# Kernel optimization log

Measured on AMD Instinct MI355X. Metric: run time of the kernel, lower is better.

The kernel has to match this reference:

```python
import jax, jax.numpy as jnp
import numpy as np

NUM_LONGTERM_MEM = 16  # config.num_longterm_mem


def setup_inputs() -> dict:
    key = jax.random.key(0)
    ks = jax.random.split(key, 9)
    B, T, C, H = 32, 2048, 768, 1536
    s = 0.02
    return {
        "x": jax.random.normal(ks[0], (B, T, C), jnp.float32),
        "Wq": jax.random.normal(ks[1], (C, C), jnp.float32) * s,
        "bq": jax.random.normal(ks[2], (C,), jnp.float32) * s,
        "W0": jax.random.normal(ks[3], (B, H, C), jnp.float32) * s,
        "b0": jax.random.normal(ks[4], (B, H), jnp.float32) * s,
        "W1": jax.random.normal(ks[5], (B, C, H), jnp.float32) * s,
        "b1": jax.random.normal(ks[6], (B, C), jnp.float32) * s,
        "Wo": jax.random.normal(ks[7], (C, C), jnp.float32) * s,
        "bo": jax.random.normal(ks[8], (C,), jnp.float32) * s,
    }


def reference(x, Wq, bq, W0, b0, W1, b1, Wo, bo):
    # x: [B, T, C]. Per-sample memory MLP weights W0 [B,H,C], W1 [B,C,H].
    B, T, C = x.shape
    L = NUM_LONGTERM_MEM
    # query projection (nn.Linear: x @ W^T + b)
    q = jnp.einsum("btc,dc->btd", x, Wq) + bq                       # [B,T,C]
    # per-sample 2-layer memory MLP with SiLU
    h = jax.nn.silu(jnp.einsum("btc,bhc->bth", q, W0) + b0[:, None, :])  # [B,T,H]
    mem = jnp.einsum("bth,bch->btc", h, W1) + b1[:, None, :]        # [B,T,C]
    # adaptive_avg_pool1d over T -> L (T divisible by L => uniform window mean)
    pooled = mem.reshape(B, L, T // L, C).mean(axis=2)              # [B,L,C]
    # output projection
    return jnp.einsum("blc,dc->bld", pooled, Wo) + bo               # [B,L,C]
```

## Files before the change

### kernel.cpp

```cpp
#include <hip/hip_runtime.h>
#include <stdint.h>

#define B_ 32
#define T_ 2048
#define C_ 768
#define H_ 1536
#define L_ 16

typedef unsigned short u16;
typedef __bf16 bf16x8 __attribute__((ext_vector_type(8)));
typedef float f32x4 __attribute__((ext_vector_type(4)));

__device__ __forceinline__ u16 f2bf(float f) {
    union { float f; uint32_t u; } v; v.f = f;
    uint32_t r = (v.u + 0x7fffu + ((v.u >> 16) & 1u)) >> 16;
    return (u16)r;
}

__device__ __forceinline__ float wave_sum(float v) {
    v += __shfl_xor(v, 1);  v += __shfl_xor(v, 2);  v += __shfl_xor(v, 4);
    v += __shfl_xor(v, 8);  v += __shfl_xor(v, 16); v += __shfl_xor(v, 32);
    return v;
}

__global__ void k_cvt(const float* __restrict__ in, u16* __restrict__ out, int n4) {
    int stride = gridDim.x * blockDim.x;
    for (int i = blockIdx.x * blockDim.x + threadIdx.x; i < n4; i += stride) {
        float4 v = reinterpret_cast<const float4*>(in)[i];
        ushort4 o;
        o.x = f2bf(v.x); o.y = f2bf(v.y); o.z = f2bf(v.z); o.w = f2bf(v.w);
        reinterpret_cast<ushort4*>(out)[i] = o;
    }
}

__global__ void k_cvt3(const float* __restrict__ s0, u16* __restrict__ d0, int n0,
                       const float* __restrict__ s1, u16* __restrict__ d1, int n1,
                       const float* __restrict__ s2, u16* __restrict__ d2, int n2,
                       int e0, int e1) {
    const float* s; u16* d; int n, b0, nb;
    if (blockIdx.x < (unsigned)e0)      { s = s0; d = d0; n = n0; b0 = 0;  nb = e0; }
    else if (blockIdx.x < (unsigned)e1) { s = s1; d = d1; n = n1; b0 = e0; nb = e1 - e0; }
    else                      { s = s2; d = d2; n = n2; b0 = e1; nb = gridDim.x - e1; }
    int stride = nb * blockDim.x;
    for (int i = (blockIdx.x - b0) * blockDim.x + threadIdx.x; i < n; i += stride) {
        float4 v = reinterpret_cast<const float4*>(s)[i];
        ushort4 o;
        o.x = f2bf(v.x); o.y = f2bf(v.y); o.z = f2bf(v.z); o.w = f2bf(v.w);
        reinterpret_cast<ushort4*>(d)[i] = o;
    }
}

__device__ __forceinline__ void gload16(const u16* g, u16* l) {
    __builtin_amdgcn_global_load_lds((const __attribute__((address_space(1))) void*)g,
                                     (__attribute__((address_space(3))) void*)l, 16, 0, 0);
}

template <int EPI>
__global__ __launch_bounds__(512, 2) void k_gemm9(const u16* __restrict__ Aall,
                                                  const u16* __restrict__ Ball,
                                                  const float* __restrict__ biasall,
                                                  u16* __restrict__ qout,
                                                  float* __restrict__ ph) {
    __shared__ u16 sm[81920];
    const int t = threadIdx.x;
    const int w = t >> 6, lane = t & 63;
    const int wr = w >> 2, wc = w & 3;
    const int l15 = lane & 15, kq = lane >> 4, cx = lane & 7;

    const int gx = gridDim.x, gy = gridDim.y;
    const int nwg = gx * gy * gridDim.z;
    int flat = blockIdx.x + gx * (blockIdx.y + gy * blockIdx.z);
    if ((nwg & 7) == 0) flat = (flat & 7) * (nwg >> 3) + (flat >> 3);
    const int bx = flat % gx;
    const int tmp = flat / gx;
    const int by = tmp % gy;
    const int bz = tmp / gy;

    const int n0 = bx * 256;
    const int m0 = by * 256;
    const u16* A; const u16* Bm; const float* bias;
    if constexpr (EPI == 0) {
        A = Aall + (size_t)m0 * C_;
        Bm = Ball + (size_t)n0 * C_;
        bias = biasall + n0;
    } else {
        A = Aall + ((size_t)bz * T_ + m0) * C_;
        Bm = Ball + ((size_t)bz * H_ + n0) * C_;
        bias = biasall + (size_t)bz * H_ + n0;
    }

    const int rl = (w << 4) + (lane >> 3);
    const int cs = (((lane & 7) ^ ((lane >> 3) & 7)) << 3);
    const int ldst = (w << 10);

    auto stA = [&](int kt, int buf) {
#pragma unroll
        for (int h = 0; h < 2; ++h) {
            const u16* g = A + (size_t)(h * 128 + rl) * C_ + kt * 64 + cs;
            u16* l = sm + buf * 16384 + h * 8192 + ldst;
            gload16(g, l);
            gload16(g + 8 * C_, l + 512);
        }
    };
    auto stB = [&](int kt, int buf) {
#pragma unroll
        for (int h = 0; h < 2; ++h) {
            const u16* g = Bm + (size_t)(h * 128 + rl) * C_ + kt * 64 + cs;
            u16* l = sm + 49152 + buf * 16384 + h * 8192 + ldst;
            gload16(g, l);
            gload16(g + 8 * C_, l + 512);
        }
    };

    f32x4 acc[8][4];
#pragma unroll
    for (int m = 0; m < 8; ++m)
#pragma unroll
        for (int n = 0; n < 4; ++n) acc[m][n] = (f32x4){0.f, 0.f, 0.f, 0.f};

    bf16x8 a0[4][2], a1[4][2], bfr[2][2];

    const int koff0 = ((kq ^ cx) << 3);
    const int koff1 = (((4 + kq) ^ cx) << 3);
    const u16* aB0 = sm + wr * 8192 + l15 * 64 + koff0;
    const u16* aB1 = sm + wr * 8192 + l15 * 64 + koff1;
    const u16* bB0 = sm + 49152 + (wc >> 1) * 8192 + (wc & 1) * 4096 + l15 * 64 + koff0;
    const u16* bB1 = sm + 49152 + (wc >> 1) * 8192 + (wc & 1) * 4096 + l15 * 64 + koff1;

    auto rdB0 = [&](int off) {
        bfr[0][0] = *reinterpret_cast<const bf16x8*>(bB0 + off);
        bfr[1][0] = *reinterpret_cast<const bf16x8*>(bB0 + off + 1024);
        bfr[0][1] = *reinterpret_cast<const bf16x8*>(bB1 + off);
        bfr[1][1] = *reinterpret_cast<const bf16x8*>(bB1 + off + 1024);
    };
    auto rdB1 = [&](int off) {
        bfr[0][0] = *reinterpret_cast<const bf16x8*>(bB0 + off + 2048);
        bfr[1][0] = *reinterpret_cast<const bf16x8*>(bB0 + off + 3072);
        bfr[0][1] = *reinterpret_cast<const bf16x8*>(bB1 + off + 2048);
        bfr[1][1] = *reinterpret_cast<const bf16x8*>(bB1 + off + 3072);
    };
    auto rdA0 = [&](int off) {
#pragma unroll
        for (int mm = 0; mm < 4; ++mm) {
            a0[mm][0] = *reinterpret_cast<const bf16x8*>(aB0 + off + mm * 1024);
            a0[mm][1] = *reinterpret_cast<const bf16x8*>(aB1 + off + mm * 1024);
        }
    };
    auto rdA1 = [&](int off) {
#pragma unroll
        for (int mm = 0; mm < 4; ++mm) {
            a1[mm][0] = *reinterpret_cast<const bf16x8*>(aB0 + off + 4096 + mm * 1024);
            a1[mm][1] = *reinterpret_cast<const bf16x8*>(aB1 + off + 4096 + mm * 1024);
        }
    };
    auto mma16 = [&](bf16x8 (&a)[4][2], int mq, int qn) {
        __builtin_amdgcn_s_setprio(1);
#pragma unroll
        for (int ks = 0; ks < 2; ++ks)
#pragma unroll
            for (int mm = 0; mm < 4; ++mm)
#pragma unroll
                for (int nn = 0; nn < 2; ++nn)
                    acc[mq * 4 + mm][qn * 2 + nn] = __builtin_amdgcn_mfma_f32_16x16x32_bf16(
                        a[mm][ks], bfr[nn][ks], acc[mq * 4 + mm][qn * 2 + nn], 0, 0, 0);
        __builtin_amdgcn_s_setprio(0);
    };

    stA(0, 0); stB(0, 0); stA(1, 1);
    asm volatile("s_waitcnt vmcnt(4)" ::: "memory");
    __builtin_amdgcn_s_barrier();

    int ba = 0;
#pragma unroll 1
    for (int kt = 0; kt < 12; ++kt) {
        const int bb = kt & 1;
        int ban = ba + 2; if (ban >= 3) ban -= 3;
        const bool s2 = (kt + 2 < 12);
        if (kt + 1 < 12) stB(kt + 1, bb ^ 1);
        if (s2) stA(kt + 2, ban);
        const int aoff = ba * 16384;
        const int boff = bb * 16384;
        rdB0(boff);
        rdA0(aoff);
        rdA1(aoff);
        mma16(a0, 0, 0);
        mma16(a1, 1, 0);
        __builtin_amdgcn_sched_barrier(0);
        rdB1(boff);
        mma16(a0, 0, 1);
        mma16(a1, 1, 1);
        if (s2) asm volatile("s_waitcnt vmcnt(4)" ::: "memory");
        else    asm volatile("s_waitcnt vmcnt(0)" ::: "memory");
        __builtin_amdgcn_s_barrier();
        ba = (ba + 1 == 3) ? 0 : ba + 1;
    }

    if constexpr (EPI == 0) {
        const int colb = n0 + wc * 64 + l15;
        const int rowb = m0 + wr * 128 + (kq << 2);
        float bv[4];
#pragma unroll
        for (int n = 0; n < 4; ++n) bv[n] = bias[wc * 64 + n * 16 + l15];
#pragma unroll
        for (int m = 0; m < 8; ++m)
#pragma unroll
            for (int r = 0; r < 4; ++r) {
                size_t ro = (size_t)(rowb + m * 16 + r) * C_;
#pragma unroll
                for (int n = 0; n < 4; ++n)
                    qout[ro + colb + n * 16] = f2bf(acc[m][n][r] + bv[n]);
            }
    } else {
        const int lwin = by * 2 + wr;
#pragma unroll
        for (int n = 0; n < 4; ++n) {
            int cloc = wc * 64 + n * 16 + l15;
            float bv = bias[cloc];
            float s = 0.f;
#pragma unroll
            for (int m = 0; m < 8; ++m)
#pragma unroll
                for (int r = 0; r < 4; ++r) {
                    float v = acc[m][n][r] + bv;
                    s += v / (1.f + __expf(-v));
                }
            s += __shfl_xor(s, 16);
            s += __shfl_xor(s, 32);
            if (kq == 0)
                ph[((size_t)bz * L_ + lwin) * H_ + n0 + cloc] = s * (1.f / 128.f);
        }
    }
}

__device__ __forceinline__ void stage_bf16_gload(const u16* gtile, int ld, u16* Ts,
                                                 int w, int lane) {
    const int r_in = lane >> 3;
    const int c0   = (lane & 7) << 3;
#pragma unroll
    for (int j = 0; j < 4; ++j) {
        int row = ((w << 2) + j) * 8 + r_in;
        const u16* g = gtile + (size_t)row * ld + c0;
        u16* l = Ts + (((w << 2) + j) << 9);
        gload16(g, l);
    }
}

__device__ __forceinline__ void stage_f32_cvt(const float* gtile, int ld, u16* Ts, int t) {
#pragma unroll
    for (int i = 0; i < 8; ++i) {
        int slot = t + (i << 8);
        int row  = slot >> 4;
        int c4   = (slot & 15) << 2;
        float4 v = *reinterpret_cast<const float4*>(gtile + (size_t)row * ld + c4);
        ushort4 o;
        o.x = f2bf(v.x); o.y = f2bf(v.y); o.z = f2bf(v.z); o.w = f2bf(v.w);
        *reinterpret_cast<ushort4*>(&Ts[row * 64 + c4]) = o;
    }
}

__device__ __forceinline__ void mfma_tile(const u16* As, const u16* Bs,
                                          f32x4 (&acc)[4][4], int wr, int wc, int lane) {
#pragma unroll
    for (int ks = 0; ks < 2; ++ks) {
        const int ko = (ks << 5) + ((lane >> 4) << 3);
        bf16x8 a[4], b[4];
#pragma unroll
        for (int m = 0; m < 4; ++m)
            a[m] = *reinterpret_cast<const bf16x8*>(&As[(wr * 64 + m * 16 + (lane & 15)) * 64 + ko]);
#pragma unroll
        for (int n = 0; n < 4; ++n)
            b[n] = *reinterpret_cast<const bf16x8*>(&Bs[(wc * 64 + n * 16 + (lane & 15)) * 64 + ko]);
#pragma unroll
        for (int m = 0; m < 4; ++m)
#pragma unroll
            for (int n = 0; n < 4; ++n)
                acc[m][n] = __builtin_amdgcn_mfma_f32_16x16x32_bf16(a[m], b[n], acc[m][n], 0, 0, 0);
    }
}

__global__ __launch_bounds__(256, 2) void k_gemm1(const float* __restrict__ x,
                                                  const u16* __restrict__ Wqb,
                                                  const float* __restrict__ bq,
                                                  u16* __restrict__ qb) {
    __shared__ u16 As[128 * 64];
    __shared__ u16 Bs[128 * 64];
    const int t = threadIdx.x, w = t >> 6, lane = t & 63;
    const int wr = w >> 1, wc = w & 1;
    const int m0 = blockIdx.y * 128;
    const int n0 = blockIdx.x * 128;

    f32x4 acc[4][4];
#pragma unroll
    for (int m = 0; m < 4; ++m)
#pragma unroll
        for (int n = 0; n < 4; ++n) acc[m][n] = (f32x4){0.f, 0.f, 0.f, 0.f};

    for (int kt = 0; kt < C_ / 64; ++kt) {
        stage_f32_cvt(x + (size_t)m0 * C_ + kt * 64, C_, As, t);
        stage_bf16_gload(Wqb + (size_t)n0 * C_ + kt * 64, C_, Bs, w, lane);
        __syncthreads();
        mfma_tile(As, Bs, acc, wr, wc, lane);
        __syncthreads();
    }

    const int r0 = m0 + wr * 64 + ((lane >> 4) << 2);
    const int cb = n0 + wc * 64 + (lane & 15);
#pragma unroll
    for (int n = 0; n < 4; ++n) {
        int c = cb + n * 16;
        float bb = bq[c];
#pragma unroll
        for (int m = 0; m < 4; ++m)
#pragma unroll
            for (int r = 0; r < 4; ++r)
                qb[(size_t)(r0 + m * 16 + r) * C_ + c] = f2bf(acc[m][n][r] + bb);
    }
}

template <bool BPRE>
__global__ __launch_bounds__(256, 2) void k_gemm2(const u16* __restrict__ qb,
                                                  const u16* __restrict__ W0b,
                                                  const float* __restrict__ W0f,
                                                  const float* __restrict__ b0,
                                                  float* __restrict__ ph) {
    __shared__ u16 As[128 * 64];
    __shared__ u16 Bs[128 * 64];
    __shared__ float Ps[2][128];
    const int t = threadIdx.x, w = t >> 6, lane = t & 63;
    const int wr = w >> 1, wc = w & 1;
    const int b  = blockIdx.z;
    const int mt = blockIdx.y;
    const int n0 = blockIdx.x * 128;
    const u16* Abase = qb + ((size_t)b * T_ + mt * 128) * C_;

    f32x4 acc[4][4];
#pragma unroll
    for (int m = 0; m < 4; ++m)
#pragma unroll
        for (int n = 0; n < 4; ++n) acc[m][n] = (f32x4){0.f, 0.f, 0.f, 0.f};

    for (int kt = 0; kt < C_ / 64; ++kt) {
        stage_bf16_gload(Abase + kt * 64, C_, As, w, lane);
        if (BPRE)
            stage_bf16_gload(W0b + ((size_t)b * H_ + n0) * C_ + kt * 64, C_, Bs, w, lane);
        else
            stage_f32_cvt(W0f + ((size_t)b * H_ + n0) * C_ + kt * 64, C_, Bs, t);
        __syncthreads();
        mfma_tile(As, Bs, acc, wr, wc, lane);
        __syncthreads();
    }

    float s[4];
#pragma unroll
    for (int n = 0; n < 4; ++n) {
        int c = n0 + wc * 64 + n * 16 + (lane & 15);
        float bb = b0[b * H_ + c];
        float sum = 0.f;
#pragma unroll
        for (int m = 0; m < 4; ++m)
#pragma unroll
            for (int r = 0; r < 4; ++r) {
                float v = acc[m][n][r] + bb;
                sum += v / (1.f + __expf(-v));
            }
        sum += __shfl_xor(sum, 16);
        sum += __shfl_xor(sum, 32);
        s[n] = sum;
    }
    if (lane < 16) {
#pragma unroll
        for (int n = 0; n < 4; ++n) Ps[wr][wc * 64 + n * 16 + lane] = s[n];
    }
    __syncthreads();
    if (t < 128)
        ph[((size_t)b * L_ + mt) * H_ + n0 + t] = (Ps[0][t] + Ps[1][t]) * (1.f / 128.f);
}

__global__ __launch_bounds__(256) void k_3a(const float* __restrict__ ph,
                                            const float* __restrict__ W1,
                                            const float* __restrict__ b1,
                                            float* __restrict__ pooled) {
    const int t = threadIdx.x, w = t >> 6, lane = t & 63;
    const int b  = blockIdx.y;
    const int cb = blockIdx.x * 16 + w * 4;

    float acc[4][16];
#pragma unroll
    for (int g = 0; g < 4; ++g)
#pragma unroll
        for (int l = 0; l < 16; ++l) acc[g][l] = 0.f;

    for (int i = 0; i < H_ / 256; ++i) {
        int h0 = i * 256 + lane * 4;
        float4 wv[4];
#pragma unroll
        for (int g = 0; g < 4; ++g)
            wv[g] = *reinterpret_cast<const float4*>(W1 + ((size_t)b * C_ + cb + g) * H_ + h0);
#pragma unroll
        for (int l = 0; l < 16; ++l) {
            float4 pv = *reinterpret_cast<const float4*>(ph + ((size_t)b * L_ + l) * H_ + h0);
#pragma unroll
            for (int g = 0; g < 4; ++g)
                acc[g][l] += wv[g].x * pv.x + wv[g].y * pv.y + wv[g].z * pv.z + wv[g].w * pv.w;
        }
    }
#pragma unroll
    for (int g = 0; g < 4; ++g)
#pragma unroll
        for (int l = 0; l < 16; ++l) acc[g][l] = wave_sum(acc[g][l]);

    if (lane < 16) {
#pragma unroll
        for (int g = 0; g < 4; ++g)
            pooled[((size_t)b * L_ + lane) * C_ + cb + g] = acc[g][lane] + b1[b * C_ + cb + g];
    }
}

__global__ __launch_bounds__(256) void k_3b(const float* __restrict__ pooled,
                                            const float* __restrict__ Wo,
                                            const float* __restrict__ bo,
                                            float* __restrict__ out) {
    __shared__ __align__(16) float ps[4 * 768];
    const int t = threadIdx.x, w = t >> 6, lane = t & 63;
    const int rr0 = blockIdx.x * 4;

    for (int idx = t; idx < 4 * 768; idx += 256)
        ps[idx] = pooled[(size_t)rr0 * 768 + idx];
    __syncthreads();

    for (int d = w; d < 768; d += 4) {
        float a0 = 0.f, a1 = 0.f, a2 = 0.f, a3 = 0.f;
#pragma unroll
        for (int i = 0; i < 3; ++i) {
            int c = i * 256 + lane * 4;
            float4 wv = *reinterpret_cast<const float4*>(Wo + (size_t)d * 768 + c);
            float4 p0 = *reinterpret_cast<const float4*>(&ps[0 * 768 + c]);
            float4 p1 = *reinterpret_cast<const float4*>(&ps[1 * 768 + c]);
            float4 p2 = *reinterpret_cast<const float4*>(&ps[2 * 768 + c]);
            float4 p3 = *reinterpret_cast<const float4*>(&ps[3 * 768 + c]);
            a0 += wv.x * p0.x + wv.y * p0.y + wv.z * p0.z + wv.w * p0.w;
            a1 += wv.x * p1.x + wv.y * p1.y + wv.z * p1.z + wv.w * p1.w;
            a2 += wv.x * p2.x + wv.y * p2.y + wv.z * p2.z + wv.w * p2.w;
            a3 += wv.x * p3.x + wv.y * p3.y + wv.z * p3.z + wv.w * p3.w;
        }
        a0 = wave_sum(a0); a1 = wave_sum(a1); a2 = wave_sum(a2); a3 = wave_sum(a3);
        if (lane == 0) {
            float bb = bo[d];
            out[(size_t)(rr0 + 0) * 768 + d] = a0 + bb;
            out[(size_t)(rr0 + 1) * 768 + d] = a1 + bb;
            out[(size_t)(rr0 + 2) * 768 + d] = a2 + bb;
            out[(size_t)(rr0 + 3) * 768 + d] = a3 + bb;
        }
    }
}

extern "C" void kernel_launch(void* const* d_in, const int* in_sizes, int n_in,
                              void* d_out, int out_size, void* d_ws, size_t ws_size,
                              hipStream_t stream) {
    const float* x  = (const float*)d_in[0];
    const float* Wq = (const float*)d_in[1];
    const float* bq = (const float*)d_in[2];
    const float* W0 = (const float*)d_in[3];
    const float* b0 = (const float*)d_in[4];
    const float* W1 = (const float*)d_in[5];
    const float* b1 = (const float*)d_in[6];
    const float* Wo = (const float*)d_in[7];
    const float* bo = (const float*)d_in[8];
    float* out = (float*)d_out;

    char* p = (char*)d_ws;
    size_t off = 0;
    auto carve = [&](size_t bytes) -> char* {
        char* r = p + off;
        off += (bytes + 255) & ~(size_t)255;
        return r;
    };
    u16*   qb     = (u16*)carve((size_t)B_ * T_ * C_ * 2);
    u16*   Wqb    = (u16*)carve((size_t)C_ * C_ * 2);
    float* ph     = (float*)carve((size_t)B_ * L_ * H_ * 4);
    float* pooled = (float*)carve((size_t)B_ * L_ * C_ * 4);

    const size_t xb_bytes  = (size_t)B_ * T_ * C_ * 2;
    const size_t w0b_bytes = (size_t)B_ * H_ * C_ * 2;

    const int n4x  = B_ * T_ * C_ / 4;
    const int n4wq = C_ * C_ / 4;
    const int n4w0 = B_ * H_ * C_ / 4;

    if (off + xb_bytes + w0b_bytes <= ws_size) {
        u16* xb  = (u16*)carve(xb_bytes);
        u16* W0b = (u16*)carve(w0b_bytes);
        k_cvt3<<<dim3(3072), 256, 0, stream>>>(x, xb, n4x, Wq, Wqb, n4wq,
                                               W0, W0b, n4w0, 1744, 1768);
        k_gemm9<0><<<dim3(C_ / 256, (B_ * T_) / 256), 512, 0, stream>>>(xb, Wqb, bq, qb, nullptr);
        k_gemm9<1><<<dim3(H_ / 256, T_ / 256, B_), 512, 0, stream>>>(qb, W0b, b0, nullptr, ph);
    } else if (off + xb_bytes <= ws_size) {
        u16* xb  = (u16*)carve(xb_bytes);
        u16* W0b = xb;
        k_cvt3<<<dim3(3072), 256, 0, stream>>>(x, xb, n4x, Wq, Wqb, n4wq,
                                               nullptr, nullptr, 0, 3040, 3072);
        k_gemm9<0><<<dim3(C_ / 256, (B_ * T_) / 256), 512, 0, stream>>>(xb, Wqb, bq, qb, nullptr);
        k_cvt<<<dim3(2048), 256, 0, stream>>>(W0, W0b, n4w0);
        k_gemm9<1><<<dim3(H_ / 256, T_ / 256, B_), 512, 0, stream>>>(qb, W0b, b0, nullptr, ph);
    } else {
        u16* W0b = nullptr;
        if (off + w0b_bytes <= ws_size) W0b = (u16*)carve(w0b_bytes);

        k_cvt<<<dim3(64), 256, 0, stream>>>(Wq, Wqb, n4wq);
        if (W0b)
            k_cvt<<<dim3(2048), 256, 0, stream>>>(W0, W0b, n4w0);
        k_gemm1<<<dim3(C_ / 128, (B_ * T_) / 128), 256, 0, stream>>>(x, Wqb, bq, qb);
        if (W0b)
            k_gemm2<true><<<dim3(H_ / 128, L_, B_), 256, 0, stream>>>(qb, W0b, nullptr, b0, ph);
        else
            k_gemm2<false><<<dim3(H_ / 128, L_, B_), 256, 0, stream>>>(qb, nullptr, W0, b0, ph);
    }

    k_3a<<<dim3(C_ / 16, B_), 256, 0, stream>>>(ph, W1, b1, pooled);
    k_3b<<<dim3(B_ * L_ / 4), 256, 0, stream>>>(pooled, Wo, bo, out);
}
```

Before: 623.8 us.

## Fold query projection into per-sample W0 to skip the q GEMM

Uses associativity to precompute Wf = W0·Wq per sample and b0' = b0 + W0·bq. The first layer then runs directly on x, so the large B·T×C×C query GEMM and the q round-trip through memory go away. The price is a new per-sample C×C weight-fusion GEMM (B·H·C·C), a transposed Wq copy, and extra workspace for Wfb. Rounding Wf to bf16 also changes the numerics slightly.

```diff
diff --git a/kernel.cpp b/kernel.cpp
--- a/kernel.cpp
+++ b/kernel.cpp
@@ -33,20 +33,60 @@
     }
 }
 
-__global__ void k_cvt3(const float* __restrict__ s0, u16* __restrict__ d0, int n0,
-                       const float* __restrict__ s1, u16* __restrict__ d1, int n1,
-                       const float* __restrict__ s2, u16* __restrict__ d2, int n2,
-                       int e0, int e1) {
-    const float* s; u16* d; int n, b0, nb;
-    if (blockIdx.x < (unsigned)e0)      { s = s0; d = d0; n = n0; b0 = 0;  nb = e0; }
-    else if (blockIdx.x < (unsigned)e1) { s = s1; d = d1; n = n1; b0 = e0; nb = e1 - e0; }
-    else                      { s = s2; d = d2; n = n2; b0 = e1; nb = gridDim.x - e1; }
-    int stride = nb * blockDim.x;
-    for (int i = (blockIdx.x - b0) * blockDim.x + threadIdx.x; i < n; i += stride) {
-        float4 v = reinterpret_cast<const float4*>(s)[i];
-        ushort4 o;
-        o.x = f2bf(v.x); o.y = f2bf(v.y); o.z = f2bf(v.z); o.w = f2bf(v.w);
-        reinterpret_cast<ushort4*>(d)[i] = o;
+__global__ void k_prep(const float* __restrict__ x, u16* __restrict__ xb, int n4x,
+                       const float* __restrict__ Wq, u16* __restrict__ WqTb,
+                       const float* __restrict__ W0, u16* __restrict__ W0b,
+                       const float* __restrict__ bq, const float* __restrict__ b0,
+                       float* __restrict__ b0f, int e0, int e1) {
+    const int t = threadIdx.x;
+    if (blockIdx.x < (unsigned)e0) {
+        int stride = e0 * 256;
+        for (int i = blockIdx.x * 256 + t; i < n4x; i += stride) {
+            float4 v = reinterpret_cast<const float4*>(x)[i];
+            ushort4 o;
+            o.x = f2bf(v.x); o.y = f2bf(v.y); o.z = f2bf(v.z); o.w = f2bf(v.w);
+            reinterpret_cast<ushort4*>(xb)[i] = o;
+        }
+    } else if (blockIdx.x < (unsigned)e1) {
+        __shared__ u16 tl[64 * 65];
+        const int nb = e1 - e0;
+        for (int tile = blockIdx.x - e0; tile < 144; tile += nb) {
+            int d0 = (tile / 12) * 64, c0 = (tile % 12) * 64;
+            __syncthreads();
+#pragma unroll
+            for (int p = 0; p < 16; ++p) {
+                int idx = p * 256 + t;
+                int r = idx >> 6, c = idx & 63;
+                tl[r * 65 + c] = f2bf(Wq[(size_t)(d0 + r) * 768 + c0 + c]);
+            }
+            __syncthreads();
+#pragma unroll
+            for (int p = 0; p < 16; ++p) {
+                int idx = p * 256 + t;
+                int r = idx >> 6, c = idx & 63;
+                WqTb[(size_t)(c0 + r) * 768 + d0 + c] = tl[c * 65 + r];
+            }
+        }
+    } else {
+        const int w = t >> 6, lane = t & 63;
+        const int nWaves = (gridDim.x - e1) * 4;
+        const float4* bq4 = reinterpret_cast<const float4*>(bq);
+        for (int rr = (blockIdx.x - e1) * 4 + w; rr < B_ * H_; rr += nWaves) {
+            const float4* src = reinterpret_cast<const float4*>(W0 + (size_t)rr * 768);
+            ushort4* dst = reinterpret_cast<ushort4*>(W0b + (size_t)rr * 768);
+            float dot = 0.f;
+#pragma unroll
+            for (int p = 0; p < 3; ++p) {
+                float4 v = src[p * 64 + lane];
+                float4 b4 = bq4[p * 64 + lane];
+                ushort4 o;
+                o.x = f2bf(v.x); o.y = f2bf(v.y); o.z = f2bf(v.z); o.w = f2bf(v.w);
+                dst[p * 64 + lane] = o;
+                dot += v.x * b4.x + v.y * b4.y + v.z * b4.z + v.w * b4.w;
+            }
+            dot = wave_sum(dot);
+            if (lane == 0) b0f[rr] = b0[rr] + dot;
+        }
     }
 }
 
@@ -232,6 +272,155 @@
     }
 }
 
+__global__ __launch_bounds__(512, 2) void k_wf(const u16* __restrict__ W0b,
+                                               const u16* __restrict__ WqTb,
+                                               u16* __restrict__ Wfb) {
+    __shared__ u16 sm[81920];
+    const int t = threadIdx.x;
+    const int w = t >> 6, lane = t & 63;
+    const int wr = w >> 2, wc = w & 3;
+    const int l15 = lane & 15, kq = lane >> 4, cx = lane & 7;
+
+    const int gx = gridDim.x, gy = gridDim.y;
+    const int nwg = gx * gy * gridDim.z;
+    int flat = blockIdx.x + gx * (blockIdx.y + gy * blockIdx.z);
+    if ((nwg & 7) == 0) flat = (flat & 7) * (nwg >> 3) + (flat >> 3);
+    const int bx = flat % gx;
+    const int tmp = flat / gx;
+    const int by = tmp % gy;
+    const int bz = tmp / gy;
+
+    const int n0 = bx * 256;
+    const int m0 = by * 256;
+    const u16* A = W0b + ((size_t)bz * H_ + m0) * C_;
+    const u16* Bm = WqTb + (size_t)n0 * C_;
+
+    const int rl = (w << 4) + (lane >> 3);
+    const int cs = (((lane & 7) ^ ((lane >> 3) & 7)) << 3);
+    const int ldst = (w << 10);
+
+    auto stA = [&](int kt, int buf) {
+#pragma unroll
+        for (int h = 0; h < 2; ++h) {
+            const u16* g = A + (size_t)(h * 128 + rl) * C_ + kt * 64 + cs;
+            u16* l = sm + buf * 16384 + h * 8192 + ldst;
+            gload16(g, l);
+            gload16(g + 8 * C_, l + 512);
+        }
+    };
+    auto stB = [&](int kt, int buf) {
+#pragma unroll
+        for (int h = 0; h < 2; ++h) {
+            const u16* g = Bm + (size_t)(h * 128 + rl) * C_ + kt * 64 + cs;
+            u16* l = sm + 49152 + buf * 16384 + h * 8192 + ldst;
+            gload16(g, l);
+            gload16(g + 8 * C_, l + 512);
+        }
+    };
+
+    f32x4 acc[8][4];
+#pragma unroll
+    for (int m = 0; m < 8; ++m)
+#pragma unroll
+        for (int n = 0; n < 4; ++n) acc[m][n] = (f32x4){0.f, 0.f, 0.f, 0.f};
+
+    bf16x8 a0[4][2], a1[4][2], bfr[2][2];
+
+    const int koff0 = ((kq ^ cx) << 3);
+    const int koff1 = (((4 + kq) ^ cx) << 3);
+    const u16* aB0 = sm + wr * 8192 + l15 * 64 + koff0;
+    const u16* aB1 = sm + wr * 8192 + l15 * 64 + koff1;
+    const u16* bB0 = sm + 49152 + (wc >> 1) * 8192 + (wc & 1) * 4096 + l15 * 64 + koff0;
+    const u16* bB1 = sm + 49152 + (wc >> 1) * 8192 + (wc & 1) * 4096 + l15 * 64 + koff1;
+
+    auto rdB0 = [&](int off) {
+        bfr[0][0] = *reinterpret_cast<const bf16x8*>(bB0 + off);
+        bfr[1][0] = *reinterpret_cast<const bf16x8*>(bB0 + off + 1024);
+        bfr[0][1] = *reinterpret_cast<const bf16x8*>(bB1 + off);
+        bfr[1][1] = *reinterpret_cast<const bf16x8*>(bB1 + off + 1024);
+    };
+    auto rdB1 = [&](int off) {
+        bfr[0][0] = *reinterpret_cast<const bf16x8*>(bB0 + off + 2048);
+        bfr[1][0] = *reinterpret_cast<const bf16x8*>(bB0 + off + 3072);
+        bfr[0][1] = *reinterpret_cast<const bf16x8*>(bB1 + off + 2048);
+        bfr[1][1] = *reinterpret_cast<const bf16x8*>(bB1 + off + 3072);
+    };
+    auto rdA0 = [&](int off) {
+#pragma unroll
+        for (int mm = 0; mm < 4; ++mm) {
+            a0[mm][0] = *reinterpret_cast<const bf16x8*>(aB0 + off + mm * 1024);
+            a0[mm][1] = *reinterpret_cast<const bf16x8*>(aB1 + off + mm * 1024);
+        }
+    };
+    auto rdA1 = [&](int off) {
+#pragma unroll
+        for (int mm = 0; mm < 4; ++mm) {
+            a1[mm][0] = *reinterpret_cast<const bf16x8*>(aB0 + off + 4096 + mm * 1024);
+            a1[mm][1] = *reinterpret_cast<const bf16x8*>(aB1 + off + 4096 + mm * 1024);
+        }
+    };
+    auto mma16 = [&](bf16x8 (&a)[4][2], int mq, int qn) {
+        __builtin_amdgcn_s_setprio(1);
+#pragma unroll
+        for (int ks = 0; ks < 2; ++ks)
+#pragma unroll
+            for (int mm = 0; mm < 4; ++mm)
+#pragma unroll
+                for (int nn = 0; nn < 2; ++nn)
+                    acc[mq * 4 + mm][qn * 2 + nn] = __builtin_amdgcn_mfma_f32_16x16x32_bf16(
+                        a[mm][ks], bfr[nn][ks], acc[mq * 4 + mm][qn * 2 + nn], 0, 0, 0);
+        __builtin_amdgcn_s_setprio(0);
+    };
+
+    stA(0, 0); stB(0, 0); stA(1, 1);
+    asm volatile("s_waitcnt vmcnt(4)" ::: "memory");
+    __builtin_amdgcn_s_barrier();
+
+    int ba = 0;
+#pragma unroll 1
+    for (int kt = 0; kt < 12; ++kt) {
+        const int bb = kt & 1;
+        int ban = ba + 2; if (ban >= 3) ban -= 3;
+        const bool s2 = (kt + 2 < 12);
+        if (kt + 1 < 12) stB(kt + 1, bb ^ 1);
+        if (s2) stA(kt + 2, ban);
+        const int aoff = ba * 16384;
+        const int boff = bb * 16384;
+        rdB0(boff);
+        rdA0(aoff);
+        rdA1(aoff);
+        mma16(a0, 0, 0);
+        mma16(a1, 1, 0);
+        __builtin_amdgcn_sched_barrier(0);
+        rdB1(boff);
+        mma16(a0, 0, 1);
+        mma16(a1, 1, 1);
+        if (s2) asm volatile("s_waitcnt vmcnt(4)" ::: "memory");
+        else    asm volatile("s_waitcnt vmcnt(0)" ::: "memory");
+        __builtin_amdgcn_s_barrier();
+        ba = (ba + 1 == 3) ? 0 : ba + 1;
+    }
+
+    const int lr0 = wr * 128 + (kq << 2);
+    const int lc0 = wc * 64 + l15;
+#pragma unroll
+    for (int m = 0; m < 8; ++m)
+#pragma unroll
+        for (int n = 0; n < 4; ++n)
+#pragma unroll
+            for (int r = 0; r < 4; ++r)
+                sm[(lr0 + m * 16 + r) * 264 + lc0 + n * 16] = f2bf(acc[m][n][r]);
+    __builtin_amdgcn_s_barrier();
+    u16* G = Wfb + ((size_t)bz * H_ + m0) * C_ + n0;
+#pragma unroll
+    for (int p = 0; p < 16; ++p) {
+        int fl = p * 512 + t;
+        int row = fl >> 5, c8 = fl & 31;
+        f32x4 v = *reinterpret_cast<const f32x4*>(&sm[row * 264 + c8 * 8]);
+        *reinterpret_cast<f32x4*>(&G[(size_t)row * C_ + c8 * 8]) = v;
+    }
+}
+
 __device__ __forceinline__ void stage_bf16_gload(const u16* gtile, int ld, u16* Ts,
                                                  int w, int lane) {
     const int r_in = lane >> 3;
@@ -475,45 +664,52 @@
         off += (bytes + 255) & ~(size_t)255;
         return r;
     };
-    u16*   qb     = (u16*)carve((size_t)B_ * T_ * C_ * 2);
-    u16*   Wqb    = (u16*)carve((size_t)C_ * C_ * 2);
     float* ph     = (float*)carve((size_t)B_ * L_ * H_ * 4);
     float* pooled = (float*)carve((size_t)B_ * L_ * C_ * 4);
 
     const size_t xb_bytes  = (size_t)B_ * T_ * C_ * 2;
     const size_t w0b_bytes = (size_t)B_ * H_ * C_ * 2;
+    const size_t wq_bytes  = (size_t)C_ * C_ * 2;
+    const size_t b0f_bytes = (size_t)B_ * H_ * 4;
 
     const int n4x  = B_ * T_ * C_ / 4;
     const int n4wq = C_ * C_ / 4;
     const int n4w0 = B_ * H_ * C_ / 4;
 
-    if (off + xb_bytes + w0b_bytes <= ws_size) {
-        u16* xb  = (u16*)carve(xb_bytes);
-        u16* W0b = (u16*)carve(w0b_bytes);
-        k_cvt3<<<dim3(3072), 256, 0, stream>>>(x, xb, n4x, Wq, Wqb, n4wq,
-                                               W0, W0b, n4w0, 1744, 1768);
-        k_gemm9<0><<<dim3(C_ / 256, (B_ * T_) / 256), 512, 0, stream>>>(xb, Wqb, bq, qb, nullptr);
-        k_gemm9<1><<<dim3(H_ / 256, T_ / 256, B_), 512, 0, stream>>>(qb, W0b, b0, nullptr, ph);
-    } else if (off + xb_bytes <= ws_size) {
-        u16* xb  = (u16*)carve(xb_bytes);
-        u16* W0b = xb;
-        k_cvt3<<<dim3(3072), 256, 0, stream>>>(x, xb, n4x, Wq, Wqb, n4wq,
-                                               nullptr, nullptr, 0, 3040, 3072);
-        k_gemm9<0><<<dim3(C_ / 256, (B_ * T_) / 256), 512, 0, stream>>>(xb, Wqb, bq, qb, nullptr);
-        k_cvt<<<dim3(2048), 256, 0, stream>>>(W0, W0b, n4w0);
-        k_gemm9<1><<<dim3(H_ / 256, T_ / 256, B_), 512, 0, stream>>>(qb, W0b, b0, nullptr, ph);
+    if (off + b0f_bytes + wq_bytes + xb_bytes + w0b_bytes + w0b_bytes <= ws_size) {
+        float* b0f  = (float*)carve(b0f_bytes);
+        u16*   WqTb = (u16*)carve(wq_bytes);
+        u16*   xb   = (u16*)carve(xb_bytes);
+        u16*   W0b  = (u16*)carve(w0b_bytes);
+        u16*   Wfb  = (u16*)carve(w0b_bytes);
+
+        k_prep<<<dim3(3072), 256, 0, stream>>>(x, xb, n4x, Wq, WqTb, W0, W0b,
+                                               bq, b0, b0f, 1872, 1896);
+        k_wf<<<dim3(C_ / 256, H_ / 256, B_), 512, 0, stream>>>(W0b, WqTb, Wfb);
+        k_gemm9<1><<<dim3(H_ / 256, T_ / 256, B_), 512, 0, stream>>>(xb, Wfb, b0f, nullptr, ph);
     } else {
-        u16* W0b = nullptr;
-        if (off + w0b_bytes <= ws_size) W0b = (u16*)carve(w0b_bytes);
-
-        k_cvt<<<dim3(64), 256, 0, stream>>>(Wq, Wqb, n4wq);
-        if (W0b)
+        u16* qb  = (u16*)carve((size_t)B_ * T_ * C_ * 2);
+        u16* Wqb = (u16*)carve(wq_bytes);
+        if (off + xb_bytes <= ws_size) {
+            u16* xb  = (u16*)carve(xb_bytes);
+            u16* W0b = xb;
+            k_cvt<<<dim3(64), 256, 0, stream>>>(Wq, Wqb, n4wq);
+            k_cvt<<<dim3(2048), 256, 0, stream>>>(x, xb, n4x);
+            k_gemm9<0><<<dim3(C_ / 256, (B_ * T_) / 256), 512, 0, stream>>>(xb, Wqb, bq, qb, nullptr);
             k_cvt<<<dim3(2048), 256, 0, stream>>>(W0, W0b, n4w0);
-        k_gemm1<<<dim3(C_ / 128, (B_ * T_) / 128), 256, 0, stream>>>(x, Wqb, bq, qb);
-        if (W0b)
-            k_gemm2<true><<<dim3(H_ / 128, L_, B_), 256, 0, stream>>>(qb, W0b, nullptr, b0, ph);
-        else
-            k_gemm2<false><<<dim3(H_ / 128, L_, B_), 256, 0, stream>>>(qb, nullptr, W0, b0, ph);
+            k_gemm9<1><<<dim3(H_ / 256, T_ / 256, B_), 512, 0, stream>>>(qb, W0b, b0, nullptr, ph);
+        } else {
+            u16* W0b = nullptr;
+            if (off + w0b_bytes <= ws_size) W0b = (u16*)carve(w0b_bytes);
+            k_cvt<<<dim3(64), 256, 0, stream>>>(Wq, Wqb, n4wq);
+            if (W0b)
+                k_cvt<<<dim3(2048), 256, 0, stream>>>(W0, W0b, n4w0);
+            k_gemm1<<<dim3(C_ / 128, (B_ * T_) / 128), 256, 0, stream>>>(x, Wqb, bq, qb);
+            if (W0b)
+                k_gemm2<true><<<dim3(H_ / 128, L_, B_), 256, 0, stream>>>(qb, W0b, nullptr, b0, ph);
+            else
+                k_gemm2<false><<<dim3(H_ / 128, L_, B_), 256, 0, stream>>>(qb, nullptr, W0, b0, ph);
+        }
     }
 
     k_3a<<<dim3(C_ / 16, B_), 256, 0, stream>>>(ph, W1, b1, pooled);
```

Measured after the change: 620.0 us. No clear change (-0.6%).
